# Performance work log

Hardware: AMD Instinct MI355X
Metric: run time of the kernel (lower is better)

The kernel has to match this reference:

```python
import jax, jax.numpy as jnp
import numpy as np

N, E, F_IN, D, X_DIM, T_DIM = 5000, 80000, 32, 64, 3, 6
P1, P2, H = 256, 32, 256
LOG_SCALE = 1.4763057  # sqrt(c) * 1.4763057 with c=1; Euclidean logmap0 is identity
W_DATA, W_PDE, W_ENT = 1.0, 1.0, 1.0

def time_encode(t):
    k_lin = T_DIM // 2
    k_log = T_DIM - k_lin
    s_lin = 10.0 ** jnp.arange(2, 2 * T_DIM, 1, dtype=jnp.float32)
    s_log = 10.0 ** jnp.arange(-2, 2 * T_DIM, 1, dtype=jnp.float32)
    t_lin = (t / jnp.clip(s_lin, 1e-7))[:k_lin]
    t_log = jnp.log((t / jnp.clip(s_log, 1e-7))[:k_log] + 1.0)
    return jnp.concatenate([t_lin, t_log])

def _forward(x0, adj, t, y, W_enc, W_pool1, W_pool2, W_emb1, W_emb2, W1, b1, W2, b2):
    t0 = t[0]
    # ---- encode: encoder + Euclidean log-map scaling ----
    z_x = jnp.tanh(x0 @ W_enc)                      # [N, D+X_DIM]
    z = z_x[:, :-X_DIM] * LOG_SCALE                 # [N, D]
    x_sp = 0.0 * z_x[:, -X_DIM:]                    # eps = 0 as in encode()
    t_enc = time_encode(t0)                         # [T_DIM]
    tx = jnp.concatenate([t_enc[None, :] * jnp.ones((N, 1)), x_sp], axis=-1)  # [N, T_DIM+X_DIM]
    # ---- renorm: dense adjacency scatter + DiffPool-style coarsening ----
    A = jnp.zeros((N, N), dtype=x0.dtype).at[adj[0], adj[1]].set(1.0)
    x = z
    y_cur = y                                        # [1, N]
    z_r = z
    y_r = y
    loss_ent = 0.0
    for Wp, We in ((W_pool1, W_emb1), (W_pool2, W_emb2)):
        S = jax.nn.softmax((x @ Wp) * LOG_SCALE, axis=0)        # [m, n] soft assignment
        m, n = S.shape
        ze = jnp.tanh(A @ (x @ We))                             # GNN embed at this level
        x = jnp.einsum('ij,ik->jk', S, ze) * (n / m)            # pooled features [n, D]
        y_cur = jnp.einsum('ij,ki->kj', S, y_cur) * (n / m)     # pooled targets [1, n]
        A = jnp.einsum('ji,jk,kl->il', S, A, S)                 # S^T A S -> [n, n]
        z_r = jnp.concatenate([z_r, x], axis=0)
        y_r = jnp.concatenate([y_r, y_cur], axis=-1)
        loss_ent = loss_ent + jax.scipy.special.entr(S).mean()
    M = z_r.shape[0]                                 # N + P1 + P2
    tx_all = tx[0] * jnp.ones((M, 1))                # broadcast first row -> [M, T_DIM+X_DIM]
    # ---- decoder + val_grad_lap: nested jacfwd Hessian diagonal ----
    def decode(txz):
        h = jnp.tanh(txz @ W1 + b1)
        return h @ W2 + b2                           # [1]
    def vgl(tx_i, z_i):
        def f(tx_):
            u = decode(jnp.concatenate([tx_, z_i]))
            return u, u
        def vg(tx_):
            g, u = jax.jacfwd(f, has_aux=True)(tx_)
            return g, (g, u)
        g2, (g, u) = jax.jacfwd(vg, has_aux=True)(tx_i)  # [1, d, d]
        hess = jax.vmap(jnp.diag)(g2)                     # [1, d]
        lap = hess[:, 1:].sum(1)                          # [1]
        return u, g, lap
    u, grad, lap = jax.vmap(vgl)(tx_all, z_r)        # [M,1], [M,1,d], [M,1]
    red = u.sum(-1)                                   # reduction -> [M]
    loss_data = jnp.mean(jnp.square(red - y_r[0]))
    res = grad[:, 0, 0] - lap[:, 0]                   # heat-equation residual u_t - lap
    loss_pde = jnp.mean(jnp.square(res))
    return W_DATA * loss_data + W_PDE * loss_pde + W_ENT * loss_ent

def setup_inputs():
    key = jax.random.key(0)
    ks = jax.random.split(key, 13)
    d_tx = T_DIM + X_DIM
    return {
        'x0': jax.random.normal(ks[0], (N, F_IN), dtype=jnp.float32),
        'adj': jax.random.randint(ks[1], (2, E), 0, N),
        't': jax.random.uniform(ks[2], (1,), dtype=jnp.float32) * 100.0,
        'y': jax.random.normal(ks[3], (1, N), dtype=jnp.float32),
        'W_enc': 0.2 * jax.random.normal(ks[4], (F_IN, D + X_DIM), dtype=jnp.float32),
        'W_pool1': 0.2 * jax.random.normal(ks[5], (D, P1), dtype=jnp.float32),
        'W_pool2': 0.2 * jax.random.normal(ks[6], (D, P2), dtype=jnp.float32),
        'W_emb1': 0.1 * jax.random.normal(ks[7], (D, D), dtype=jnp.float32),
        'W_emb2': 0.1 * jax.random.normal(ks[8], (D, D), dtype=jnp.float32),
        'W1': 0.1 * jax.random.normal(ks[9], (d_tx + D, H), dtype=jnp.float32),
        'b1': 0.01 * jax.random.normal(ks[10], (H,), dtype=jnp.float32),
        'W2': 0.1 * jax.random.normal(ks[11], (H, 1), dtype=jnp.float32),
        'b2': jnp.zeros((1,), dtype=jnp.float32),
    }

def reference(x0, adj, t, y, W_enc, W_pool1, W_pool2, W_emb1, W_emb2, W1, b1, W2, b2):
    return _forward(x0, adj, t, y, W_enc, W_pool1, W_pool2, W_emb1, W_emb2, W1, b1, W2, b2)
```

## Files before the change

kernel.cpp:

```cpp
#include <hip/hip_runtime.h>
#include <math.h>

#define NN 5000
#define EE 80000
#define FIN 32
#define DD 64
#define XD 3
#define TD 6
#define PP1 256
#define PP2 32
#define HH 256
#define MM (NN + PP1 + PP2)
#define CAP 64
#define NTILES 79
#define LOG_SCALE 1.4763057f
#define Y2SCALE (256.f / 5000.f)

#define A2CH 40
#define X2CH 79

#define ACC_OFF   0u
#define CNT_OFF   64u
#define DEG_OFF   256u
#define Y2A_OFF   20256u
#define X2_OFF    21280u
#define A2_OFF    86816u
#define BM_OFF    348960u
#define ZERO_BYTES 3473960u
#define PART_OFF  348960u
#define XW2_OFF   760608u
#define S2_OFF    826144u
#define ZE2_OFF   858912u
#define X3_OFF    924448u
#define Y3_OFF    932640u
#define BUCK_OFF  3473984u
#define ZEP_OFF   4753984u
#define Z_OFF     6033984u
#define S1_OFF    7313984u
#define AS1_OFF   12433984u
#define CQ_OFF    17553984u
#define DRES_OFF  17556032u
#define PA2_OFF   17598336u
#define PX2_OFF   28084096u
#define WS_ROOMY  33261504u

__device__ __forceinline__ float bsum256(float v, float* red) {
    int t = threadIdx.x;
    red[t] = v; __syncthreads();
    #pragma unroll
    for (int o = 128; o > 0; o >>= 1) {
        if (t < o) red[t] += red[t + o];
        __syncthreads();
    }
    float r = red[0]; __syncthreads();
    return r;
}

__global__ __launch_bounds__(256) void stage0(
        const float* __restrict__ x0, const float* __restrict__ Wenc,
        float* __restrict__ z,
        const int* __restrict__ adj, unsigned int* __restrict__ mask,
        int* __restrict__ bucket, int* __restrict__ deg,
        const float* __restrict__ t, const float* __restrict__ W1,
        const float* __restrict__ b1, float* __restrict__ cq) {
    __shared__ float smem[FIN * DD + 4 * FIN];
    int b = blockIdx.x;
    int tid = threadIdx.x;
    if (b < 1250) {
        float (*wx)[DD] = (float(*)[DD])smem;
        float (*xr)[FIN] = (float(*)[FIN])(smem + FIN * DD);
        int i0 = b << 2;
        int j = tid & 63;
        #pragma unroll
        for (int m = 0; m < 8; ++m) {
            int k = (tid >> 6) + (m << 2);
            wx[k][j] = Wenc[k * (DD + XD) + j];
        }
        if (tid < 128) xr[tid >> 5][tid & 31] = x0[(i0 + (tid >> 5)) * FIN + (tid & 31)];
        __syncthreads();
        int r = tid >> 6;
        float s = 0.f;
        #pragma unroll
        for (int k = 0; k < FIN; ++k) s = fmaf(xr[r][k], wx[k][j], s);
        z[(i0 + r) * DD + j] = tanhf(s) * LOG_SCALE;
    } else if (b < 1563) {
        int e = (b - 1250) * 256 + tid;
        if (e < EE) {
            int i = adj[e], jj = adj[EE + e];
            unsigned int key = (unsigned int)(i * NN + jj);
            unsigned int bit = 1u << (key & 31u);
            unsigned int old = atomicOr(&mask[key >> 5], bit);
            if (!(old & bit)) {
                int slot = atomicAdd(&deg[i], 1);
                if (slot < CAP) bucket[i * CAP + slot] = jj;
            }
        }
    } else {
        float* te = smem;
        int h = tid;
        if (h == 0) {
            float t0 = t[0];
            te[0] = t0 / 1e2f;
            te[1] = t0 / 1e3f;
            te[2] = t0 / 1e4f;
            te[3] = logf(t0 * 100.f + 1.f);
            te[4] = logf(t0 * 10.f + 1.f);
            te[5] = logf(t0 + 1.f);
        }
        __syncthreads();
        float c = b1[h];
        #pragma unroll
        for (int j2 = 0; j2 < TD; ++j2) c = fmaf(te[j2], W1[j2 * HH + h], c);
        float q = 0.f;
        #pragma unroll
        for (int j2 = 1; j2 < TD + XD; ++j2) { float w = W1[j2 * HH + h]; q = fmaf(w, w, q); }
        cq[h] = c;
        cq[HH + h] = q;
    }
}

__global__ __launch_bounds__(256) void stage1(
        const float* __restrict__ z, const float* __restrict__ Wp1,
        float* __restrict__ S1, float* __restrict__ part,
        const int* __restrict__ bucket, const int* __restrict__ deg,
        const float* __restrict__ We1, float* __restrict__ zep) {
    __shared__ float smem[2 * 64 * 64];
    int b = blockIdx.x;
    int tid = threadIdx.x;
    if (b < NTILES * 4) {
        float (*sa)[64] = (float(*)[64])smem;
        float (*sb)[64] = (float(*)[64])(smem + 4096);
        int tm = (b >> 2) << 6;
        int tn = (b & 3) << 6;
        int r0 = tid >> 4, c0 = (tid & 15) << 2;
        const float4 zero4 = make_float4(0.f, 0.f, 0.f, 0.f);
        #pragma unroll
        for (int m = 0; m < 4; ++m) {
            int row = r0 + (m << 4);
            int gr = tm + row;
            *(float4*)&sa[row][c0] = (gr < NN) ? *(const float4*)&z[gr * DD + c0] : zero4;
            *(float4*)&sb[row][c0] = *(const float4*)&Wp1[row * PP1 + tn + c0];
        }
        __syncthreads();
        int tx = (tid & 15) << 2;
        int ty = (tid >> 4) << 2;
        float acc[4][4] = {};
        #pragma unroll
        for (int kk = 0; kk < 64; ++kk) {
            float a0 = sa[ty + 0][kk];
            float a1 = sa[ty + 1][kk];
            float a2 = sa[ty + 2][kk];
            float a3 = sa[ty + 3][kk];
            float4 bv = *(const float4*)&sb[kk][tx];
            acc[0][0] = fmaf(a0, bv.x, acc[0][0]);
            acc[0][1] = fmaf(a0, bv.y, acc[0][1]);
            acc[0][2] = fmaf(a0, bv.z, acc[0][2]);
            acc[0][3] = fmaf(a0, bv.w, acc[0][3]);
            acc[1][0] = fmaf(a1, bv.x, acc[1][0]);
            acc[1][1] = fmaf(a1, bv.y, acc[1][1]);
            acc[1][2] = fmaf(a1, bv.z, acc[1][2]);
            acc[1][3] = fmaf(a1, bv.w, acc[1][3]);
            acc[2][0] = fmaf(a2, bv.x, acc[2][0]);
            acc[2][1] = fmaf(a2, bv.y, acc[2][1]);
            acc[2][2] = fmaf(a2, bv.z, acc[2][2]);
            acc[2][3] = fmaf(a2, bv.w, acc[2][3]);
            acc[3][0] = fmaf(a3, bv.x, acc[3][0]);
            acc[3][1] = fmaf(a3, bv.y, acc[3][1]);
            acc[3][2] = fmaf(a3, bv.z, acc[3][2]);
            acc[3][3] = fmaf(a3, bv.w, acc[3][3]);
        }
        #pragma unroll
        for (int i2 = 0; i2 < 4; ++i2)
            #pragma unroll
            for (int j = 0; j < 4; ++j) acc[i2][j] *= LOG_SCALE;
        #pragma unroll
        for (int i2 = 0; i2 < 4; ++i2) {
            int gr = tm + ty + i2;
            if (gr < NN)
                *(float4*)&S1[gr * PP1 + tn + tx] =
                    make_float4(acc[i2][0], acc[i2][1], acc[i2][2], acc[i2][3]);
        }
        int nvalid = NN - (tm + ty);
        nvalid = (nvalid < 0) ? 0 : (nvalid > 4 ? 4 : nvalid);
        float vm[4], vs[4];
        #pragma unroll
        for (int j = 0; j < 4; ++j) {
            float m = -3.0e38f;
            #pragma unroll
            for (int i2 = 0; i2 < 4; ++i2) if (i2 < nvalid) m = fmaxf(m, acc[i2][j]);
            float s = 0.f;
            #pragma unroll
            for (int i2 = 0; i2 < 4; ++i2) if (i2 < nvalid) s += expf(acc[i2][j] - m);
            vm[j] = m; vs[j] = s;
        }
        __syncthreads();
        float* redm = smem;
        float* reds = smem + 1024;
        int g = tid >> 4;
        #pragma unroll
        for (int j = 0; j < 4; ++j) {
            redm[g * 64 + tx + j] = vm[j];
            reds[g * 64 + tx + j] = vs[j];
        }
        __syncthreads();
        if (tid < 64) {
            float M = -3.0e38f, S = 0.f;
            #pragma unroll
            for (int g2 = 0; g2 < 16; ++g2) {
                float m2 = redm[g2 * 64 + tid], s2 = reds[g2 * 64 + tid];
                float Mn = fmaxf(M, m2);
                S = S * expf(M - Mn) + s2 * expf(m2 - Mn);
                M = Mn;
            }
            int rt = tm >> 6;
            part[rt * 512 + tn + tid] = M;
            part[rt * 512 + 256 + tn + tid] = S;
        }
    } else {
        float (*zs)[DD] = (float(*)[DD])smem;
        int w = tid >> 6, d = tid & 63;
        int i = ((b - NTILES * 4) << 2) + w;
        int n = min(deg[i], CAP);
        const int* bk = bucket + i * CAP;
        float a0 = 0.f, a1 = 0.f, a2 = 0.f, a3 = 0.f;
        int s = 0;
        for (; s + 4 <= n; s += 4) {
            a0 += z[bk[s] * DD + d];
            a1 += z[bk[s + 1] * DD + d];
            a2 += z[bk[s + 2] * DD + d];
            a3 += z[bk[s + 3] * DD + d];
        }
        for (; s < n; ++s) a0 += z[bk[s] * DD + d];
        zs[w][d] = (a0 + a1) + (a2 + a3);
        __syncthreads();
        float acc = 0.f;
        #pragma unroll
        for (int k = 0; k < DD; ++k) acc = fmaf(zs[w][k], We1[k * DD + d], acc);
        zep[i * DD + d] = tanhf(acc);
    }
}

__global__ void smax_norm(float* __restrict__ S, const float* __restrict__ part,
                          const float* __restrict__ y, float* __restrict__ y2acc,
                          float* __restrict__ ent) {
    __shared__ float red[256];
    __shared__ float ybuf[4][64];
    __shared__ float cst[64];
    int rt = blockIdx.x % NTILES, ct = blockIdx.x / NTILES;
    int lc = threadIdx.x & 63, q = threadIdx.x >> 6;
    int c = (ct << 6) + lc;
    float M = -3.0e38f, Sv = 0.f;
    for (int ch = q; ch < NTILES; ch += 4) {
        float m2 = part[ch * 512 + c];
        float s2 = part[ch * 512 + 256 + c];
        float Mn = fmaxf(M, m2);
        Sv = Sv * expf(M - Mn) + s2 * expf(m2 - Mn);
        M = Mn;
    }
    red[threadIdx.x] = M; ybuf[q][lc] = Sv;
    __syncthreads();
    if (q == 0) {
        float Mm = red[lc], Ss = ybuf[0][lc];
        #pragma unroll
        for (int g = 1; g < 4; ++g) {
            float m2 = red[g * 64 + lc], s2 = ybuf[g][lc];
            float Mn = fmaxf(Mm, m2);
            Ss = Ss * expf(Mm - Mn) + s2 * expf(m2 - Mn);
            Mm = Mn;
        }
        cst[lc] = Mm + logf(Ss);
    }
    __syncthreads();
    float mxlns = cst[lc];
    float en = 0.f, ys = 0.f;
    #pragma unroll
    for (int k = 0; k < 16; ++k) {
        int r = (rt << 6) + (k << 2) + q;
        if (r < NN) {
            float v = S[r * PP1 + c];
            float s = expf(v - mxlns);
            S[r * PP1 + c] = s;
            en += s * (mxlns - v);
            ys = fmaf(s, y[r], ys);
        }
    }
    __syncthreads();
    ybuf[q][lc] = ys;
    en = bsum256(en, red);
    if (threadIdx.x == 0) atomicAdd(ent, en);
    if (q == 0) atomicAdd(&y2acc[c], ybuf[0][lc] + ybuf[1][lc] + ybuf[2][lc] + ybuf[3][lc]);
}

__global__ void gather_as(const int* __restrict__ bucket, const int* __restrict__ deg,
                          const float* __restrict__ S1, float* __restrict__ AS1) {
    int i = blockIdx.x, c = threadIdx.x;
    int n = min(deg[i], CAP);
    const int* bk = bucket + i * CAP;
    float a0 = 0.f, a1 = 0.f, a2 = 0.f, a3 = 0.f;
    int s = 0;
    for (; s + 4 <= n; s += 4) {
        a0 += S1[bk[s] * PP1 + c];
        a1 += S1[bk[s + 1] * PP1 + c];
        a2 += S1[bk[s + 2] * PP1 + c];
        a3 += S1[bk[s + 3] * PP1 + c];
    }
    for (; s < n; ++s) a0 += S1[bk[s] * PP1 + c];
    AS1[i * PP1 + c] = (a0 + a1) + (a2 + a3);
}

__global__ __launch_bounds__(256) void gemm_fused(
        const float* __restrict__ S1, const float* __restrict__ AS1,
        const float* __restrict__ zep, float* __restrict__ PA2, float* __restrict__ PX2) {
    __shared__ float sa[32][64];
    __shared__ float sb[32][64];
    int b = blockIdx.x;
    const float* B;
    float* dst;
    int tm, tn, k0, k1, NB;
    if (b < 640) {
        int tile = b & 15, chunk = b >> 4;
        tm = (tile >> 2) << 6; tn = (tile & 3) << 6;
        k0 = chunk * 128; k1 = min(k0 + 128, NN);
        B = AS1; NB = PP1;
        dst = PA2 + chunk * (PP1 * PP1);
    } else {
        int b2 = b - 640;
        int tile = b2 & 3, chunk = b2 >> 2;
        tm = tile << 6; tn = 0;
        k0 = chunk * 64; k1 = min(k0 + 64, NN);
        B = zep; NB = DD;
        dst = PX2 + chunk * (PP1 * DD);
    }
    int tid = threadIdx.x;
    int tx = (tid & 15) << 2;
    int ty = (tid >> 4) << 2;
    int r0 = tid >> 4, c0 = (tid & 15) << 2;
    int r1 = (tid + 256) >> 4, c1 = c0;
    float acc[4][4] = {};
    const float4 z4 = make_float4(0.f, 0.f, 0.f, 0.f);
    for (int kb = k0; kb < k1; kb += 32) {
        int ka0 = kb + r0, ka1 = kb + r1;
        *(float4*)&sa[r0][c0] = (ka0 < k1) ? *(const float4*)&S1[ka0 * PP1 + tm + c0] : z4;
        *(float4*)&sa[r1][c1] = (ka1 < k1) ? *(const float4*)&S1[ka1 * PP1 + tm + c1] : z4;
        *(float4*)&sb[r0][c0] = (ka0 < k1) ? *(const float4*)&B[ka0 * NB + tn + c0] : z4;
        *(float4*)&sb[r1][c1] = (ka1 < k1) ? *(const float4*)&B[ka1 * NB + tn + c1] : z4;
        __syncthreads();
        #pragma unroll
        for (int kk = 0; kk < 32; ++kk) {
            float4 av = *(const float4*)&sa[kk][ty];
            float4 bv = *(const float4*)&sb[kk][tx];
            acc[0][0] = fmaf(av.x, bv.x, acc[0][0]);
            acc[0][1] = fmaf(av.x, bv.y, acc[0][1]);
            acc[0][2] = fmaf(av.x, bv.z, acc[0][2]);
            acc[0][3] = fmaf(av.x, bv.w, acc[0][3]);
            acc[1][0] = fmaf(av.y, bv.x, acc[1][0]);
            acc[1][1] = fmaf(av.y, bv.y, acc[1][1]);
            acc[1][2] = fmaf(av.y, bv.z, acc[1][2]);
            acc[1][3] = fmaf(av.y, bv.w, acc[1][3]);
            acc[2][0] = fmaf(av.z, bv.x, acc[2][0]);
            acc[2][1] = fmaf(av.z, bv.y, acc[2][1]);
            acc[2][2] = fmaf(av.z, bv.z, acc[2][2]);
            acc[2][3] = fmaf(av.z, bv.w, acc[2][3]);
            acc[3][0] = fmaf(av.w, bv.x, acc[3][0]);
            acc[3][1] = fmaf(av.w, bv.y, acc[3][1]);
            acc[3][2] = fmaf(av.w, bv.z, acc[3][2]);
            acc[3][3] = fmaf(av.w, bv.w, acc[3][3]);
        }
        __syncthreads();
    }
    #pragma unroll
    for (int i = 0; i < 4; ++i)
        *(float4*)&dst[(tm + ty + i) * NB + tn + tx] =
            make_float4(acc[i][0], acc[i][1], acc[i][2], acc[i][3]);
}

__global__ void reduce_parts(const float* __restrict__ PA2, const float* __restrict__ PX2,
                             float* __restrict__ A2, float* __restrict__ x2) {
    int idx = blockIdx.x * 256 + threadIdx.x;
    if (idx < PP1 * PP1) {
        float s = 0.f;
        #pragma unroll 8
        for (int c = 0; c < A2CH; ++c) s += PA2[c * (PP1 * PP1) + idx];
        A2[idx] = s;
    } else {
        int e = idx - PP1 * PP1;
        float s = 0.f;
        #pragma unroll 8
        for (int c = 0; c < X2CH; ++c) s += PX2[c * (PP1 * DD) + e];
        x2[e] = s * Y2SCALE;
    }
}

__global__ void gemm_tn(const float* __restrict__ A, const float* __restrict__ B,
                        float* __restrict__ C, int M, int N, int K, int kchunk, float scale) {
    __shared__ float sa[32][64];
    __shared__ float sb[32][64];
    int tilesN = N >> 6;
    int tm = (blockIdx.x / tilesN) << 6;
    int tn = (blockIdx.x % tilesN) << 6;
    int k0 = blockIdx.y * kchunk;
    int k1 = min(k0 + kchunk, K);
    int tid = threadIdx.x;
    int tx = (tid & 15) << 2;
    int ty = (tid >> 4) << 2;
    float acc[4][4] = {};
    for (int kb = k0; kb < k1; kb += 32) {
        #pragma unroll
        for (int t = 0; t < 8; ++t) {
            int idx = tid + (t << 8);
            int r = idx >> 6, cc = idx & 63;
            int k = kb + r;
            sa[r][cc] = (k < k1) ? A[k * M + tm + cc] : 0.f;
            sb[r][cc] = (k < k1) ? B[k * N + tn + cc] : 0.f;
        }
        __syncthreads();
        #pragma unroll
        for (int kk = 0; kk < 32; ++kk) {
            float4 av = *(const float4*)&sa[kk][ty];
            float4 bv = *(const float4*)&sb[kk][tx];
            acc[0][0] = fmaf(av.x, bv.x, acc[0][0]);
            acc[0][1] = fmaf(av.x, bv.y, acc[0][1]);
            acc[0][2] = fmaf(av.x, bv.z, acc[0][2]);
            acc[0][3] = fmaf(av.x, bv.w, acc[0][3]);
            acc[1][0] = fmaf(av.y, bv.x, acc[1][0]);
            acc[1][1] = fmaf(av.y, bv.y, acc[1][1]);
            acc[1][2] = fmaf(av.y, bv.z, acc[1][2]);
            acc[1][3] = fmaf(av.y, bv.w, acc[1][3]);
            acc[2][0] = fmaf(av.z, bv.x, acc[2][0]);
            acc[2][1] = fmaf(av.z, bv.y, acc[2][1]);
            acc[2][2] = fmaf(av.z, bv.z, acc[2][2]);
            acc[2][3] = fmaf(av.z, bv.w, acc[2][3]);
            acc[3][0] = fmaf(av.w, bv.x, acc[3][0]);
            acc[3][1] = fmaf(av.w, bv.y, acc[3][1]);
            acc[3][2] = fmaf(av.w, bv.z, acc[3][2]);
            acc[3][3] = fmaf(av.w, bv.w, acc[3][3]);
        }
        __syncthreads();
    }
    #pragma unroll
    for (int i = 0; i < 4; ++i)
        #pragma unroll
        for (int j = 0; j < 4; ++j)
            atomicAdd(&C[(tm + ty + i) * N + tn + tx + j], acc[i][j] * scale);
}

__global__ void mm2_fused(const float* __restrict__ x2, const float* __restrict__ We2,
                          const float* __restrict__ Wp2, float* __restrict__ XW2,
                          float* __restrict__ S2) {
    int gid = blockIdx.x * 256 + threadIdx.x;
    if (gid < PP1 * DD) {
        int i = gid >> 6, j = gid & 63;
        float s = 0.f;
        #pragma unroll
        for (int k = 0; k < DD; ++k) s = fmaf(x2[i * DD + k], We2[k * DD + j], s);
        XW2[gid] = s;
    } else {
        int e = gid - PP1 * DD;
        int i = e >> 5, j = e & 31;
        float s = 0.f;
        #pragma unroll
        for (int k = 0; k < DD; ++k) s = fmaf(x2[i * DD + k], Wp2[k * PP2 + j], s);
        S2[e] = s * LOG_SCALE;
    }
}

__global__ void level2b(float* __restrict__ S2, float* __restrict__ ent,
                        const float* __restrict__ y2acc, float* __restrict__ y3,
                        const float* __restrict__ A2, const float* __restrict__ XW2,
                        float* __restrict__ ze2) {
    __shared__ float red[256];
    int t = threadIdx.x;
    if (blockIdx.x < PP2) {
        int p = blockIdx.x;
        float l = S2[t * PP2 + p];
        red[t] = l; __syncthreads();
        #pragma unroll
        for (int o = 128; o > 0; o >>= 1) {
            if (t < o) red[t] = fmaxf(red[t], red[t + o]);
            __syncthreads();
        }
        float mx = red[0]; __syncthreads();
        float ex = expf(l - mx);
        float sum = bsum256(ex, red);
        float lns = logf(sum), inv = 1.f / sum;
        float s = ex * inv;
        S2[t * PP2 + p] = s;
        float en = s * (mx + lns - l);
        float ys = s * y2acc[t];
        en = bsum256(en, red);
        ys = bsum256(ys, red);
        if (t == 0) {
            atomicAdd(ent, en);
            y3[p] = ys * ((32.f / 256.f) * Y2SCALE);
        }
    } else {
        int gid = (blockIdx.x - PP2) * 256 + t;
        int i = gid >> 6, j = gid & 63;
        const float* a = A2 + i * PP1;
        float s = 0.f;
        #pragma unroll 16
        for (int k = 0; k < PP1; ++k) s = fmaf(a[k], XW2[k * DD + j], s);
        ze2[gid] = tanhf(s);
    }
}

__global__ void pool_x3(const float* __restrict__ S2, const float* __restrict__ ze2,
                        float* __restrict__ x3) {
    __shared__ float pr[4][64];
    int j = blockIdx.x;
    int d = threadIdx.x & 63, q = threadIdx.x >> 6;
    float a = 0.f;
    #pragma unroll 4
    for (int i = q * 64; i < q * 64 + 64; ++i)
        a = fmaf(S2[i * PP2 + j], ze2[i * DD + d], a);
    pr[q][d] = a;
    __syncthreads();
    if (q == 0) x3[j * DD + d] = (pr[0][d] + pr[1][d] + pr[2][d] + pr[3][d]) * (32.f / 256.f);
}

__global__ __launch_bounds__(256) void decoder8(
        const float* __restrict__ z, const float* __restrict__ x2,
        const float* __restrict__ x3, const float* __restrict__ y,
        const float* __restrict__ y2acc, const float* __restrict__ y3,
        const float* __restrict__ W1, const float* __restrict__ W2,
        const float* __restrict__ b2, const float* __restrict__ cq,
        float* __restrict__ dres, int* __restrict__ cnt,
        const float* __restrict__ acc, float* __restrict__ out) {
    __shared__ float zr[8][DD];
    __shared__ float rw[8][3][4];
    __shared__ int lastflag;
    int t = threadIdx.x;
    int i0 = blockIdx.x << 3;
    #pragma unroll
    for (int e = t; e < 512; e += 256) {
        int r = e >> 6, d = e & 63;
        int i = i0 + r;
        float v;
        if (i < NN) v = z[i * DD + d];
        else if (i < NN + PP1) v = x2[(i - NN) * DD + d];
        else v = x3[(i - NN - PP1) * DD + d];
        zr[r][d] = v;
    }
    __syncthreads();
    int h = t;
    float c0 = cq[h];
    float a[8];
    #pragma unroll
    for (int r = 0; r < 8; ++r) a[r] = c0;
    #pragma unroll 8
    for (int k = 0; k < DD; ++k) {
        float w = W1[(TD + XD + k) * HH + h];
        #pragma unroll
        for (int r = 0; r < 8; ++r) a[r] = fmaf(zr[r][k], w, a[r]);
    }
    float w2h = W2[h], w1h = W1[h], qh = cq[HH + h];
    float pu[8], pg[8], pl[8];
    #pragma unroll
    for (int r = 0; r < 8; ++r) {
        float th = tanhf(a[r]);
        float g1 = 1.f - th * th;
        pu[r] = w2h * th;
        pg[r] = w2h * g1 * w1h;
        pl[r] = w2h * (-2.f * th * g1) * qh;
    }
    #pragma unroll
    for (int o = 32; o > 0; o >>= 1) {
        #pragma unroll
        for (int r = 0; r < 8; ++r) {
            pu[r] += __shfl_xor(pu[r], o);
            pg[r] += __shfl_xor(pg[r], o);
            pl[r] += __shfl_xor(pl[r], o);
        }
    }
    int wave = t >> 6, lane = t & 63;
    if (lane == 0) {
        #pragma unroll
        for (int r = 0; r < 8; ++r) {
            rw[r][0][wave] = pu[r];
            rw[r][1][wave] = pg[r];
            rw[r][2][wave] = pl[r];
        }
    }
    __syncthreads();
    if (t < 8) {
        int r = t, i = i0 + r;
        float su = rw[r][0][0] + rw[r][0][1] + rw[r][0][2] + rw[r][0][3];
        float sg = rw[r][1][0] + rw[r][1][1] + rw[r][1][2] + rw[r][1][3];
        float sl = rw[r][2][0] + rw[r][2][1] + rw[r][2][2] + rw[r][2][3];
        float u = su + b2[0];
        float yv = (i < NN) ? y[i]
                 : (i < NN + PP1) ? y2acc[i - NN] * Y2SCALE
                 : y3[i - NN - PP1];
        float du = u - yv;
        float res = sg - sl;
        dres[i * 2] = du * du;
        dres[i * 2 + 1] = res * res;
        __threadfence();
    }
    __syncthreads();
    if (t == 0) lastflag = atomicAdd(cnt, 1);
    __syncthreads();
    if (lastflag == (MM / 8) - 1) {
        __threadfence();
        float* red = (float*)zr;
        float sd = 0.f, sp = 0.f;
        for (int i = t; i < MM; i += 256) {
            sd += dres[i * 2];
            sp += dres[i * 2 + 1];
        }
        sd = bsum256(sd, red);
        sp = bsum256(sp, red);
        if (t == 0)
            out[0] = sd * (1.f / MM) + sp * (1.f / MM)
                   + acc[2] * (1.f / (float)(NN * PP1)) + acc[3] * (1.f / (float)(PP1 * PP2));
    }
}

extern "C" void kernel_launch(void* const* d_in, const int* in_sizes, int n_in,
                              void* d_out, int out_size, void* d_ws, size_t ws_size,
                              hipStream_t stream) {
    const float* x0   = (const float*)d_in[0];
    const int*   adj  = (const int*)d_in[1];
    const float* t    = (const float*)d_in[2];
    const float* y    = (const float*)d_in[3];
    const float* Wenc = (const float*)d_in[4];
    const float* Wp1  = (const float*)d_in[5];
    const float* Wp2  = (const float*)d_in[6];
    const float* We1  = (const float*)d_in[7];
    const float* We2  = (const float*)d_in[8];
    const float* W1   = (const float*)d_in[9];
    const float* b1   = (const float*)d_in[10];
    const float* W2   = (const float*)d_in[11];
    const float* b2   = (const float*)d_in[12];

    char* ws = (char*)d_ws;
    float* acc   = (float*)(ws + ACC_OFF);
    int*   cnt   = (int*)(ws + CNT_OFF);
    int*   deg   = (int*)(ws + DEG_OFF);
    float* y2acc = (float*)(ws + Y2A_OFF);
    float* x2    = (float*)(ws + X2_OFF);
    float* A2    = (float*)(ws + A2_OFF);
    unsigned int* mask = (unsigned int*)(ws + BM_OFF);
    float* part  = (float*)(ws + PART_OFF);
    float* XW2   = (float*)(ws + XW2_OFF);
    float* S2    = (float*)(ws + S2_OFF);
    float* ze2   = (float*)(ws + ZE2_OFF);
    float* x3    = (float*)(ws + X3_OFF);
    float* y3    = (float*)(ws + Y3_OFF);
    int*   buck  = (int*)(ws + BUCK_OFF);
    float* zep   = (float*)(ws + ZEP_OFF);
    float* z     = (float*)(ws + Z_OFF);
    float* S1    = (float*)(ws + S1_OFF);
    float* AS1   = (float*)(ws + AS1_OFF);
    float* cq    = (float*)(ws + CQ_OFF);
    float* dres  = (float*)(ws + DRES_OFF);
    float* PA2   = (float*)(ws + PA2_OFF);
    float* PX2   = (float*)(ws + PX2_OFF);

    hipMemsetAsync(ws, 0, ZERO_BYTES, stream);

    stage0<<<1564, 256, 0, stream>>>(x0, Wenc, z, adj, mask, buck, deg, t, W1, b1, cq);
    stage1<<<NTILES * 4 + NN / 4, 256, 0, stream>>>(z, Wp1, S1, part, buck, deg, We1, zep);
    smax_norm<<<NTILES * 4, 256, 0, stream>>>(S1, part, y, y2acc, &acc[2]);
    gather_as<<<NN, PP1, 0, stream>>>(buck, deg, S1, AS1);
    if (ws_size >= WS_ROOMY) {
        gemm_fused<<<640 + 316, 256, 0, stream>>>(S1, AS1, zep, PA2, PX2);
        reduce_parts<<<320, 256, 0, stream>>>(PA2, PX2, A2, x2);
    } else {
        gemm_tn<<<dim3(4, 32), 256, 0, stream>>>(S1, zep, x2, PP1, DD, NN, 157, Y2SCALE);
        gemm_tn<<<dim3(16, 16), 256, 0, stream>>>(S1, AS1, A2, PP1, PP1, NN, 313, 1.f);
    }
    mm2_fused<<<96, 256, 0, stream>>>(x2, We2, Wp2, XW2, S2);
    level2b<<<96, 256, 0, stream>>>(S2, &acc[3], y2acc, y3, A2, XW2, ze2);
    pool_x3<<<PP2, 256, 0, stream>>>(S2, ze2, x3);
    decoder8<<<MM / 8, 256, 0, stream>>>(z, x2, x3, y, y2acc, y3, W1, W2, b2, cq,
                                         dres, cnt, acc, (float*)d_out);
}
```

Before: 227.4 us.

## Fuse gather, GEMM, decoder and pooling stages into fewer multi-role kernels

Several kernels are merged into multi-role launches. The AS1 gather, x2 GEMM partials and decoder rows for the original nodes now share one launch, and the A2 reduction, level-2 matmuls and decoder rows for the pooled nodes are folded together. pool_x3 and the final decoder become one small tail kernel that computes x3 in shared memory and does the last-block loss reduction. The aim is to cut launch count and inter-kernel gaps, and to overlap decoder work for the 5000 base rows with the pooling GEMMs. In exchange, block roles are more heterogeneous and the 4-block tail is serial.

```diff
diff --git a/kernel.cpp b/kernel.cpp
--- a/kernel.cpp
+++ b/kernel.cpp
@@ -15,7 +15,6 @@
 #define NTILES 79
 #define LOG_SCALE 1.4763057f
 #define Y2SCALE (256.f / 5000.f)
-
 #define A2CH 40
 #define X2CH 79
 
@@ -31,7 +30,6 @@
 #define XW2_OFF   760608u
 #define S2_OFF    826144u
 #define ZE2_OFF   858912u
-#define X3_OFF    924448u
 #define Y3_OFF    932640u
 #define BUCK_OFF  3473984u
 #define ZEP_OFF   4753984u
@@ -56,294 +54,24 @@
     return r;
 }
 
-__global__ __launch_bounds__(256) void stage0(
-        const float* __restrict__ x0, const float* __restrict__ Wenc,
-        float* __restrict__ z,
-        const int* __restrict__ adj, unsigned int* __restrict__ mask,
-        int* __restrict__ bucket, int* __restrict__ deg,
-        const float* __restrict__ t, const float* __restrict__ W1,
-        const float* __restrict__ b1, float* __restrict__ cq) {
-    __shared__ float smem[FIN * DD + 4 * FIN];
-    int b = blockIdx.x;
-    int tid = threadIdx.x;
-    if (b < 1250) {
-        float (*wx)[DD] = (float(*)[DD])smem;
-        float (*xr)[FIN] = (float(*)[FIN])(smem + FIN * DD);
-        int i0 = b << 2;
-        int j = tid & 63;
-        #pragma unroll
-        for (int m = 0; m < 8; ++m) {
-            int k = (tid >> 6) + (m << 2);
-            wx[k][j] = Wenc[k * (DD + XD) + j];
-        }
-        if (tid < 128) xr[tid >> 5][tid & 31] = x0[(i0 + (tid >> 5)) * FIN + (tid & 31)];
-        __syncthreads();
-        int r = tid >> 6;
-        float s = 0.f;
-        #pragma unroll
-        for (int k = 0; k < FIN; ++k) s = fmaf(xr[r][k], wx[k][j], s);
-        z[(i0 + r) * DD + j] = tanhf(s) * LOG_SCALE;
-    } else if (b < 1563) {
-        int e = (b - 1250) * 256 + tid;
-        if (e < EE) {
-            int i = adj[e], jj = adj[EE + e];
-            unsigned int key = (unsigned int)(i * NN + jj);
-            unsigned int bit = 1u << (key & 31u);
-            unsigned int old = atomicOr(&mask[key >> 5], bit);
-            if (!(old & bit)) {
-                int slot = atomicAdd(&deg[i], 1);
-                if (slot < CAP) bucket[i * CAP + slot] = jj;
-            }
-        }
-    } else {
-        float* te = smem;
-        int h = tid;
-        if (h == 0) {
-            float t0 = t[0];
-            te[0] = t0 / 1e2f;
-            te[1] = t0 / 1e3f;
-            te[2] = t0 / 1e4f;
-            te[3] = logf(t0 * 100.f + 1.f);
-            te[4] = logf(t0 * 10.f + 1.f);
-            te[5] = logf(t0 + 1.f);
-        }
-        __syncthreads();
-        float c = b1[h];
-        #pragma unroll
-        for (int j2 = 0; j2 < TD; ++j2) c = fmaf(te[j2], W1[j2 * HH + h], c);
-        float q = 0.f;
-        #pragma unroll
-        for (int j2 = 1; j2 < TD + XD; ++j2) { float w = W1[j2 * HH + h]; q = fmaf(w, w, q); }
-        cq[h] = c;
-        cq[HH + h] = q;
-    }
-}
-
-__global__ __launch_bounds__(256) void stage1(
-        const float* __restrict__ z, const float* __restrict__ Wp1,
-        float* __restrict__ S1, float* __restrict__ part,
-        const int* __restrict__ bucket, const int* __restrict__ deg,
-        const float* __restrict__ We1, float* __restrict__ zep) {
-    __shared__ float smem[2 * 64 * 64];
-    int b = blockIdx.x;
-    int tid = threadIdx.x;
-    if (b < NTILES * 4) {
-        float (*sa)[64] = (float(*)[64])smem;
-        float (*sb)[64] = (float(*)[64])(smem + 4096);
-        int tm = (b >> 2) << 6;
-        int tn = (b & 3) << 6;
-        int r0 = tid >> 4, c0 = (tid & 15) << 2;
-        const float4 zero4 = make_float4(0.f, 0.f, 0.f, 0.f);
-        #pragma unroll
-        for (int m = 0; m < 4; ++m) {
-            int row = r0 + (m << 4);
-            int gr = tm + row;
-            *(float4*)&sa[row][c0] = (gr < NN) ? *(const float4*)&z[gr * DD + c0] : zero4;
-            *(float4*)&sb[row][c0] = *(const float4*)&Wp1[row * PP1 + tn + c0];
-        }
-        __syncthreads();
-        int tx = (tid & 15) << 2;
-        int ty = (tid >> 4) << 2;
-        float acc[4][4] = {};
-        #pragma unroll
-        for (int kk = 0; kk < 64; ++kk) {
-            float a0 = sa[ty + 0][kk];
-            float a1 = sa[ty + 1][kk];
-            float a2 = sa[ty + 2][kk];
-            float a3 = sa[ty + 3][kk];
-            float4 bv = *(const float4*)&sb[kk][tx];
-            acc[0][0] = fmaf(a0, bv.x, acc[0][0]);
-            acc[0][1] = fmaf(a0, bv.y, acc[0][1]);
-            acc[0][2] = fmaf(a0, bv.z, acc[0][2]);
-            acc[0][3] = fmaf(a0, bv.w, acc[0][3]);
-            acc[1][0] = fmaf(a1, bv.x, acc[1][0]);
-            acc[1][1] = fmaf(a1, bv.y, acc[1][1]);
-            acc[1][2] = fmaf(a1, bv.z, acc[1][2]);
-            acc[1][3] = fmaf(a1, bv.w, acc[1][3]);
-            acc[2][0] = fmaf(a2, bv.x, acc[2][0]);
-            acc[2][1] = fmaf(a2, bv.y, acc[2][1]);
-            acc[2][2] = fmaf(a2, bv.z, acc[2][2]);
-            acc[2][3] = fmaf(a2, bv.w, acc[2][3]);
-            acc[3][0] = fmaf(a3, bv.x, acc[3][0]);
-            acc[3][1] = fmaf(a3, bv.y, acc[3][1]);
-            acc[3][2] = fmaf(a3, bv.z, acc[3][2]);
-            acc[3][3] = fmaf(a3, bv.w, acc[3][3]);
-        }
-        #pragma unroll
-        for (int i2 = 0; i2 < 4; ++i2)
-            #pragma unroll
-            for (int j = 0; j < 4; ++j) acc[i2][j] *= LOG_SCALE;
-        #pragma unroll
-        for (int i2 = 0; i2 < 4; ++i2) {
-            int gr = tm + ty + i2;
-            if (gr < NN)
-                *(float4*)&S1[gr * PP1 + tn + tx] =
-                    make_float4(acc[i2][0], acc[i2][1], acc[i2][2], acc[i2][3]);
-        }
-        int nvalid = NN - (tm + ty);
-        nvalid = (nvalid < 0) ? 0 : (nvalid > 4 ? 4 : nvalid);
-        float vm[4], vs[4];
-        #pragma unroll
-        for (int j = 0; j < 4; ++j) {
-            float m = -3.0e38f;
-            #pragma unroll
-            for (int i2 = 0; i2 < 4; ++i2) if (i2 < nvalid) m = fmaxf(m, acc[i2][j]);
-            float s = 0.f;
-            #pragma unroll
-            for (int i2 = 0; i2 < 4; ++i2) if (i2 < nvalid) s += expf(acc[i2][j] - m);
-            vm[j] = m; vs[j] = s;
-        }
-        __syncthreads();
-        float* redm = smem;
-        float* reds = smem + 1024;
-        int g = tid >> 4;
-        #pragma unroll
-        for (int j = 0; j < 4; ++j) {
-            redm[g * 64 + tx + j] = vm[j];
-            reds[g * 64 + tx + j] = vs[j];
-        }
-        __syncthreads();
-        if (tid < 64) {
-            float M = -3.0e38f, S = 0.f;
-            #pragma unroll
-            for (int g2 = 0; g2 < 16; ++g2) {
-                float m2 = redm[g2 * 64 + tid], s2 = reds[g2 * 64 + tid];
-                float Mn = fmaxf(M, m2);
-                S = S * expf(M - Mn) + s2 * expf(m2 - Mn);
-                M = Mn;
-            }
-            int rt = tm >> 6;
-            part[rt * 512 + tn + tid] = M;
-            part[rt * 512 + 256 + tn + tid] = S;
-        }
-    } else {
-        float (*zs)[DD] = (float(*)[DD])smem;
-        int w = tid >> 6, d = tid & 63;
-        int i = ((b - NTILES * 4) << 2) + w;
-        int n = min(deg[i], CAP);
-        const int* bk = bucket + i * CAP;
-        float a0 = 0.f, a1 = 0.f, a2 = 0.f, a3 = 0.f;
-        int s = 0;
-        for (; s + 4 <= n; s += 4) {
-            a0 += z[bk[s] * DD + d];
-            a1 += z[bk[s + 1] * DD + d];
-            a2 += z[bk[s + 2] * DD + d];
-            a3 += z[bk[s + 3] * DD + d];
-        }
-        for (; s < n; ++s) a0 += z[bk[s] * DD + d];
-        zs[w][d] = (a0 + a1) + (a2 + a3);
-        __syncthreads();
-        float acc = 0.f;
-        #pragma unroll
-        for (int k = 0; k < DD; ++k) acc = fmaf(zs[w][k], We1[k * DD + d], acc);
-        zep[i * DD + d] = tanhf(acc);
-    }
-}
-
-__global__ void smax_norm(float* __restrict__ S, const float* __restrict__ part,
-                          const float* __restrict__ y, float* __restrict__ y2acc,
-                          float* __restrict__ ent) {
-    __shared__ float red[256];
-    __shared__ float ybuf[4][64];
-    __shared__ float cst[64];
-    int rt = blockIdx.x % NTILES, ct = blockIdx.x / NTILES;
-    int lc = threadIdx.x & 63, q = threadIdx.x >> 6;
-    int c = (ct << 6) + lc;
-    float M = -3.0e38f, Sv = 0.f;
-    for (int ch = q; ch < NTILES; ch += 4) {
-        float m2 = part[ch * 512 + c];
-        float s2 = part[ch * 512 + 256 + c];
-        float Mn = fmaxf(M, m2);
-        Sv = Sv * expf(M - Mn) + s2 * expf(m2 - Mn);
-        M = Mn;
-    }
-    red[threadIdx.x] = M; ybuf[q][lc] = Sv;
-    __syncthreads();
-    if (q == 0) {
-        float Mm = red[lc], Ss = ybuf[0][lc];
-        #pragma unroll
-        for (int g = 1; g < 4; ++g) {
-            float m2 = red[g * 64 + lc], s2 = ybuf[g][lc];
-            float Mn = fmaxf(Mm, m2);
-            Ss = Ss * expf(Mm - Mn) + s2 * expf(m2 - Mn);
-            Mm = Mn;
-        }
-        cst[lc] = Mm + logf(Ss);
-    }
-    __syncthreads();
-    float mxlns = cst[lc];
-    float en = 0.f, ys = 0.f;
-    #pragma unroll
-    for (int k = 0; k < 16; ++k) {
-        int r = (rt << 6) + (k << 2) + q;
-        if (r < NN) {
-            float v = S[r * PP1 + c];
-            float s = expf(v - mxlns);
-            S[r * PP1 + c] = s;
-            en += s * (mxlns - v);
-            ys = fmaf(s, y[r], ys);
-        }
-    }
-    __syncthreads();
-    ybuf[q][lc] = ys;
-    en = bsum256(en, red);
-    if (threadIdx.x == 0) atomicAdd(ent, en);
-    if (q == 0) atomicAdd(&y2acc[c], ybuf[0][lc] + ybuf[1][lc] + ybuf[2][lc] + ybuf[3][lc]);
-}
-
-__global__ void gather_as(const int* __restrict__ bucket, const int* __restrict__ deg,
-                          const float* __restrict__ S1, float* __restrict__ AS1) {
-    int i = blockIdx.x, c = threadIdx.x;
-    int n = min(deg[i], CAP);
-    const int* bk = bucket + i * CAP;
-    float a0 = 0.f, a1 = 0.f, a2 = 0.f, a3 = 0.f;
-    int s = 0;
-    for (; s + 4 <= n; s += 4) {
-        a0 += S1[bk[s] * PP1 + c];
-        a1 += S1[bk[s + 1] * PP1 + c];
-        a2 += S1[bk[s + 2] * PP1 + c];
-        a3 += S1[bk[s + 3] * PP1 + c];
-    }
-    for (; s < n; ++s) a0 += S1[bk[s] * PP1 + c];
-    AS1[i * PP1 + c] = (a0 + a1) + (a2 + a3);
-}
-
-__global__ __launch_bounds__(256) void gemm_fused(
-        const float* __restrict__ S1, const float* __restrict__ AS1,
-        const float* __restrict__ zep, float* __restrict__ PA2, float* __restrict__ PX2) {
-    __shared__ float sa[32][64];
-    __shared__ float sb[32][64];
-    int b = blockIdx.x;
-    const float* B;
-    float* dst;
-    int tm, tn, k0, k1, NB;
-    if (b < 640) {
-        int tile = b & 15, chunk = b >> 4;
-        tm = (tile >> 2) << 6; tn = (tile & 3) << 6;
-        k0 = chunk * 128; k1 = min(k0 + 128, NN);
-        B = AS1; NB = PP1;
-        dst = PA2 + chunk * (PP1 * PP1);
-    } else {
-        int b2 = b - 640;
-        int tile = b2 & 3, chunk = b2 >> 2;
-        tm = tile << 6; tn = 0;
-        k0 = chunk * 64; k1 = min(k0 + 64, NN);
-        B = zep; NB = DD;
-        dst = PX2 + chunk * (PP1 * DD);
-    }
+__device__ void gemm_tile(const float* Amat, const float* Bmat,
+        int tm, int tn, int k0, int k1, int NB,
+        float* dst, int atomicMode, float scale, float* smem) {
+    float (*sa)[64] = (float(*)[64])smem;
+    float (*sb)[64] = (float(*)[64])(smem + 2048);
     int tid = threadIdx.x;
     int tx = (tid & 15) << 2;
     int ty = (tid >> 4) << 2;
     int r0 = tid >> 4, c0 = (tid & 15) << 2;
-    int r1 = (tid + 256) >> 4, c1 = c0;
+    int r1 = r0 + 16;
     float acc[4][4] = {};
     const float4 z4 = make_float4(0.f, 0.f, 0.f, 0.f);
     for (int kb = k0; kb < k1; kb += 32) {
         int ka0 = kb + r0, ka1 = kb + r1;
-        *(float4*)&sa[r0][c0] = (ka0 < k1) ? *(const float4*)&S1[ka0 * PP1 + tm + c0] : z4;
-        *(float4*)&sa[r1][c1] = (ka1 < k1) ? *(const float4*)&S1[ka1 * PP1 + tm + c1] : z4;
-        *(float4*)&sb[r0][c0] = (ka0 < k1) ? *(const float4*)&B[ka0 * NB + tn + c0] : z4;
-        *(float4*)&sb[r1][c1] = (ka1 < k1) ? *(const float4*)&B[ka1 * NB + tn + c1] : z4;
+        *(float4*)&sa[r0][c0] = (ka0 < k1) ? *(const float4*)&Amat[ka0 * PP1 + tm + c0] : z4;
+        *(float4*)&sa[r1][c0] = (ka1 < k1) ? *(const float4*)&Amat[ka1 * PP1 + tm + c0] : z4;
+        *(float4*)&sb[r0][c0] = (ka0 < k1) ? *(const float4*)&Bmat[ka0 * NB + tn + c0] : z4;
+        *(float4*)&sb[r1][c0] = (ka1 < k1) ? *(const float4*)&Bmat[ka1 * NB + tn + c0] : z4;
         __syncthreads();
         #pragma unroll
         for (int kk = 0; kk < 32; ++kk) {
@@ -368,106 +96,428 @@
         }
         __syncthreads();
     }
+    if (atomicMode) {
+        #pragma unroll
+        for (int i = 0; i < 4; ++i)
+            #pragma unroll
+            for (int j = 0; j < 4; ++j)
+                atomicAdd(&dst[(tm + ty + i) * NB + tn + tx + j], acc[i][j] * scale);
+    } else {
+        #pragma unroll
+        for (int i = 0; i < 4; ++i)
+            *(float4*)&dst[(tm + ty + i) * NB + tn + tx] =
+                make_float4(acc[i][0] * scale, acc[i][1] * scale,
+                            acc[i][2] * scale, acc[i][3] * scale);
+    }
+}
+
+__device__ void decoder_rows(const float* src, const float* ysrc, float yscale, int i0,
+        const float* W1, const float* W2, const float* b2, const float* cq,
+        float* dres, float* smem) {
+    float (*zr)[DD] = (float(*)[DD])smem;
+    float (*rw)[3][4] = (float(*)[3][4])(smem + 512);
+    int t = threadIdx.x;
+    zr[t >> 6][t & 63] = src[t];
+    zr[(t >> 6) + 4][t & 63] = src[t + 256];
+    __syncthreads();
+    int h = t;
+    float c0 = cq[h];
+    float a[8];
     #pragma unroll
-    for (int i = 0; i < 4; ++i)
-        *(float4*)&dst[(tm + ty + i) * NB + tn + tx] =
-            make_float4(acc[i][0], acc[i][1], acc[i][2], acc[i][3]);
-}
-
-__global__ void reduce_parts(const float* __restrict__ PA2, const float* __restrict__ PX2,
-                             float* __restrict__ A2, float* __restrict__ x2) {
-    int idx = blockIdx.x * 256 + threadIdx.x;
-    if (idx < PP1 * PP1) {
+    for (int r = 0; r < 8; ++r) a[r] = c0;
+    #pragma unroll 8
+    for (int k = 0; k < DD; ++k) {
+        float w = W1[(TD + XD + k) * HH + h];
+        #pragma unroll
+        for (int r = 0; r < 8; ++r) a[r] = fmaf(zr[r][k], w, a[r]);
+    }
+    float w2h = W2[h], w1h = W1[h], qh = cq[HH + h];
+    float pu[8], pg[8], pl[8];
+    #pragma unroll
+    for (int r = 0; r < 8; ++r) {
+        float th = tanhf(a[r]);
+        float g1 = 1.f - th * th;
+        pu[r] = w2h * th;
+        pg[r] = w2h * g1 * w1h;
+        pl[r] = w2h * (-2.f * th * g1) * qh;
+    }
+    #pragma unroll
+    for (int o = 32; o > 0; o >>= 1) {
+        #pragma unroll
+        for (int r = 0; r < 8; ++r) {
+            pu[r] += __shfl_xor(pu[r], o);
+            pg[r] += __shfl_xor(pg[r], o);
+            pl[r] += __shfl_xor(pl[r], o);
+        }
+    }
+    int wave = t >> 6, lane = t & 63;
+    if (lane == 0) {
+        #pragma unroll
+        for (int r = 0; r < 8; ++r) {
+            rw[r][0][wave] = pu[r];
+            rw[r][1][wave] = pg[r];
+            rw[r][2][wave] = pl[r];
+        }
+    }
+    __syncthreads();
+    if (t < 8) {
+        int r = t;
+        float su = rw[r][0][0] + rw[r][0][1] + rw[r][0][2] + rw[r][0][3];
+        float sg = rw[r][1][0] + rw[r][1][1] + rw[r][1][2] + rw[r][1][3];
+        float sl = rw[r][2][0] + rw[r][2][1] + rw[r][2][2] + rw[r][2][3];
+        float u = su + b2[0];
+        float du = u - ysrc[r] * yscale;
+        float res = sg - sl;
+        dres[(i0 + r) * 2] = du * du;
+        dres[(i0 + r) * 2 + 1] = res * res;
+    }
+    __syncthreads();
+}
+
+__global__ __launch_bounds__(256) void stage0(
+        const float* __restrict__ x0, const float* __restrict__ Wenc,
+        float* __restrict__ z,
+        const int* __restrict__ adj, unsigned int* __restrict__ mask,
+        int* __restrict__ bucket, int* __restrict__ deg,
+        const float* __restrict__ t, const float* __restrict__ W1,
+        const float* __restrict__ b1, float* __restrict__ cq) {
+    __shared__ __align__(16) float smem[FIN * DD + 4 * FIN];
+    int b = blockIdx.x;
+    int tid = threadIdx.x;
+    if (b < 1250) {
+        float (*wx)[DD] = (float(*)[DD])smem;
+        float (*xr)[FIN] = (float(*)[FIN])(smem + FIN * DD);
+        int i0 = b << 2;
+        int j = tid & 63;
+        #pragma unroll
+        for (int m = 0; m < 8; ++m) {
+            int k = (tid >> 6) + (m << 2);
+            wx[k][j] = Wenc[k * (DD + XD) + j];
+        }
+        if (tid < 128) xr[tid >> 5][tid & 31] = x0[(i0 + (tid >> 5)) * FIN + (tid & 31)];
+        __syncthreads();
+        int r = tid >> 6;
+        float s = 0.f;
+        #pragma unroll
+        for (int k = 0; k < FIN; ++k) s = fmaf(xr[r][k], wx[k][j], s);
+        z[(i0 + r) * DD + j] = tanhf(s) * LOG_SCALE;
+    } else if (b < 1563) {
+        int e = (b - 1250) * 256 + tid;
+        if (e < EE) {
+            int i = adj[e], jj = adj[EE + e];
+            unsigned int key = (unsigned int)(i * NN + jj);
+            unsigned int bit = 1u << (key & 31u);
+            unsigned int old = atomicOr(&mask[key >> 5], bit);
+            if (!(old & bit)) {
+                int slot = atomicAdd(&deg[i], 1);
+                if (slot < CAP) bucket[i * CAP + slot] = jj;
+            }
+        }
+    } else {
+        float* te = smem;
+        if (tid == 0) {
+            float t0 = t[0];
+            te[0] = t0 / 1e2f;
+            te[1] = t0 / 1e3f;
+            te[2] = t0 / 1e4f;
+            te[3] = logf(t0 * 100.f + 1.f);
+            te[4] = logf(t0 * 10.f + 1.f);
+            te[5] = logf(t0 + 1.f);
+        }
+        __syncthreads();
+        int h = tid;
+        float c = b1[h];
+        #pragma unroll
+        for (int j2 = 0; j2 < TD; ++j2) c = fmaf(te[j2], W1[j2 * HH + h], c);
+        float q = 0.f;
+        #pragma unroll
+        for (int j2 = 1; j2 < TD + XD; ++j2) { float w = W1[j2 * HH + h]; q = fmaf(w, w, q); }
+        cq[h] = c;
+        cq[HH + h] = q;
+    }
+}
+
+__global__ __launch_bounds__(256) void stage1(
+        const float* __restrict__ z, const float* __restrict__ Wp1,
+        float* __restrict__ S1, float* __restrict__ part,
+        const int* __restrict__ bucket, const int* __restrict__ deg,
+        const float* __restrict__ We1, float* __restrict__ zep) {
+    __shared__ __align__(16) float smem[2 * 64 * 64];
+    int b = blockIdx.x;
+    int tid = threadIdx.x;
+    if (b < NTILES * 4) {
+        float (*sa)[64] = (float(*)[64])smem;
+        float (*sb)[64] = (float(*)[64])(smem + 4096);
+        int tm = (b >> 2) << 6;
+        int tn = (b & 3) << 6;
+        int r0 = tid >> 4, c0 = (tid & 15) << 2;
+        const float4 zero4 = make_float4(0.f, 0.f, 0.f, 0.f);
+        #pragma unroll
+        for (int m = 0; m < 4; ++m) {
+            int row = r0 + (m << 4);
+            int gr = tm + row;
+            *(float4*)&sa[row][c0] = (gr < NN) ? *(const float4*)&z[gr * DD + c0] : zero4;
+            *(float4*)&sb[row][c0] = *(const float4*)&Wp1[row * PP1 + tn + c0];
+        }
+        __syncthreads();
+        int tx = (tid & 15) << 2;
+        int ty = (tid >> 4) << 2;
+        float acr[4][4] = {};
+        #pragma unroll
+        for (int kk = 0; kk < 64; ++kk) {
+            float a0 = sa[ty + 0][kk];
+            float a1 = sa[ty + 1][kk];
+            float a2 = sa[ty + 2][kk];
+            float a3 = sa[ty + 3][kk];
+            float4 bv = *(const float4*)&sb[kk][tx];
+            acr[0][0] = fmaf(a0, bv.x, acr[0][0]);
+            acr[0][1] = fmaf(a0, bv.y, acr[0][1]);
+            acr[0][2] = fmaf(a0, bv.z, acr[0][2]);
+            acr[0][3] = fmaf(a0, bv.w, acr[0][3]);
+            acr[1][0] = fmaf(a1, bv.x, acr[1][0]);
+            acr[1][1] = fmaf(a1, bv.y, acr[1][1]);
+            acr[1][2] = fmaf(a1, bv.z, acr[1][2]);
+            acr[1][3] = fmaf(a1, bv.w, acr[1][3]);
+            acr[2][0] = fmaf(a2, bv.x, acr[2][0]);
+            acr[2][1] = fmaf(a2, bv.y, acr[2][1]);
+            acr[2][2] = fmaf(a2, bv.z, acr[2][2]);
+            acr[2][3] = fmaf(a2, bv.w, acr[2][3]);
+            acr[3][0] = fmaf(a3, bv.x, acr[3][0]);
+            acr[3][1] = fmaf(a3, bv.y, acr[3][1]);
+            acr[3][2] = fmaf(a3, bv.z, acr[3][2]);
+            acr[3][3] = fmaf(a3, bv.w, acr[3][3]);
+        }
+        #pragma unroll
+        for (int i2 = 0; i2 < 4; ++i2)
+            #pragma unroll
+            for (int j = 0; j < 4; ++j) acr[i2][j] *= LOG_SCALE;
+        #pragma unroll
+        for (int i2 = 0; i2 < 4; ++i2) {
+            int gr = tm + ty + i2;
+            if (gr < NN)
+                *(float4*)&S1[gr * PP1 + tn + tx] =
+                    make_float4(acr[i2][0], acr[i2][1], acr[i2][2], acr[i2][3]);
+        }
+        int nvalid = NN - (tm + ty);
+        nvalid = (nvalid < 0) ? 0 : (nvalid > 4 ? 4 : nvalid);
+        float vm[4], vs[4];
+        #pragma unroll
+        for (int j = 0; j < 4; ++j) {
+            float m = -3.0e38f;
+            #pragma unroll
+            for (int i2 = 0; i2 < 4; ++i2) if (i2 < nvalid) m = fmaxf(m, acr[i2][j]);
+            float s = 0.f;
+            #pragma unroll
+            for (int i2 = 0; i2 < 4; ++i2) if (i2 < nvalid) s += expf(acr[i2][j] - m);
+            vm[j] = m; vs[j] = s;
+        }
+        __syncthreads();
+        float* redm = smem;
+        float* reds = smem + 1024;
+        int g = tid >> 4;
+        #pragma unroll
+        for (int j = 0; j < 4; ++j) {
+            redm[g * 64 + tx + j] = vm[j];
+            reds[g * 64 + tx + j] = vs[j];
+        }
+        __syncthreads();
+        if (tid < 64) {
+            float M = -3.0e38f, S = 0.f;
+            #pragma unroll
+            for (int g2 = 0; g2 < 16; ++g2) {
+                float m2 = redm[g2 * 64 + tid], s2 = reds[g2 * 64 + tid];
+                float Mn = fmaxf(M, m2);
+                S = S * expf(M - Mn) + s2 * expf(m2 - Mn);
+                M = Mn;
+            }
+            int rt = tm >> 6;
+            part[rt * 512 + tn + tid] = M;
+            part[rt * 512 + 256 + tn + tid] = S;
+        }
+    } else {
+        float (*zs)[DD] = (float(*)[DD])smem;
+        int w = tid >> 6, d = tid & 63;
+        int i = ((b - NTILES * 4) << 2) + w;
+        int n = min(deg[i], CAP);
+        const int* bk = bucket + i * CAP;
+        float a0 = 0.f, a1 = 0.f, a2 = 0.f, a3 = 0.f;
+        int s = 0;
+        for (; s + 4 <= n; s += 4) {
+            a0 += z[bk[s] * DD + d];
+            a1 += z[bk[s + 1] * DD + d];
+            a2 += z[bk[s + 2] * DD + d];
+            a3 += z[bk[s + 3] * DD + d];
+        }
+        for (; s < n; ++s) a0 += z[bk[s] * DD + d];
+        zs[w][d] = (a0 + a1) + (a2 + a3);
+        __syncthreads();
+        float a = 0.f;
+        #pragma unroll
+        for (int k = 0; k < DD; ++k) a = fmaf(zs[w][k], We1[k * DD + d], a);
+        zep[i * DD + d] = tanhf(a);
+    }
+}
+
+__global__ __launch_bounds__(256) void smax_norm(
+        float* __restrict__ S, const float* __restrict__ part,
+        const float* __restrict__ y, float* __restrict__ y2acc,
+        float* __restrict__ ent) {
+    __shared__ float red[256];
+    __shared__ float ybuf[4][64];
+    __shared__ float cst[64];
+    int rt = blockIdx.x % NTILES, ct = blockIdx.x / NTILES;
+    int lc = threadIdx.x & 63, q = threadIdx.x >> 6;
+    int c = (ct << 6) + lc;
+    float M = -3.0e38f, Sv = 0.f;
+    for (int ch = q; ch < NTILES; ch += 4) {
+        float m2 = part[ch * 512 + c];
+        float s2 = part[ch * 512 + 256 + c];
+        float Mn = fmaxf(M, m2);
+        Sv = Sv * expf(M - Mn) + s2 * expf(m2 - Mn);
+        M = Mn;
+    }
+    red[threadIdx.x] = M; ybuf[q][lc] = Sv;
+    __syncthreads();
+    if (q == 0) {
+        float Mm = red[lc], Ss = ybuf[0][lc];
+        #pragma unroll
+        for (int g = 1; g < 4; ++g) {
+            float m2 = red[g * 64 + lc], s2 = ybuf[g][lc];
+            float Mn = fmaxf(Mm, m2);
+            Ss = Ss * expf(Mm - Mn) + s2 * expf(m2 - Mn);
+            Mm = Mn;
+        }
+        cst[lc] = Mm + logf(Ss);
+    }
+    __syncthreads();
+    float mxlns = cst[lc];
+    float en = 0.f, ys = 0.f;
+    #pragma unroll
+    for (int k = 0; k < 16; ++k) {
+        int r = (rt << 6) + (k << 2) + q;
+        if (r < NN) {
+            float v = S[r * PP1 + c];
+            float s = expf(v - mxlns);
+            S[r * PP1 + c] = s;
+            en += s * (mxlns - v);
+            ys = fmaf(s, y[r], ys);
+        }
+    }
+    __syncthreads();
+    ybuf[q][lc] = ys;
+    en = bsum256(en, red);
+    if (threadIdx.x == 0) atomicAdd(ent, en);
+    if (q == 0) atomicAdd(&y2acc[c], ybuf[0][lc] + ybuf[1][lc] + ybuf[2][lc] + ybuf[3][lc]);
+}
+
+__global__ __launch_bounds__(256) void fuseD(
+        const int* __restrict__ bucket, const int* __restrict__ deg,
+        const float* __restrict__ S1, float* __restrict__ AS1,
+        const float* __restrict__ zep, float* __restrict__ PX2,
+        float* __restrict__ x2,
+        const float* __restrict__ z, const float* __restrict__ y,
+        const float* __restrict__ W1, const float* __restrict__ W2,
+        const float* __restrict__ b2, const float* __restrict__ cq,
+        float* __restrict__ dres, int roomy) {
+    __shared__ __align__(16) float smem[4096];
+    int b = blockIdx.x;
+    if (b < NN) {
+        int i = b, c = threadIdx.x;
+        int n = min(deg[i], CAP);
+        const int* bk = bucket + i * CAP;
+        float a0 = 0.f, a1 = 0.f, a2 = 0.f, a3 = 0.f;
+        int s = 0;
+        for (; s + 4 <= n; s += 4) {
+            a0 += S1[bk[s] * PP1 + c];
+            a1 += S1[bk[s + 1] * PP1 + c];
+            a2 += S1[bk[s + 2] * PP1 + c];
+            a3 += S1[bk[s + 3] * PP1 + c];
+        }
+        for (; s < n; ++s) a0 += S1[bk[s] * PP1 + c];
+        AS1[i * PP1 + c] = (a0 + a1) + (a2 + a3);
+    } else if (b < NN + 316) {
+        int vb2 = b - NN;
+        int tile = vb2 & 3, chunk = vb2 >> 2;
+        int k0 = chunk * 64, k1 = min(k0 + 64, NN);
+        float* dst = roomy ? (PX2 + chunk * (PP1 * DD)) : x2;
+        gemm_tile(S1, zep, tile << 6, 0, k0, k1, DD, dst, 1 - roomy,
+                  roomy ? 1.f : Y2SCALE, smem);
+    } else {
+        int r8 = b - (NN + 316);
+        decoder_rows(z + (r8 << 3) * DD, y + (r8 << 3), 1.f, r8 << 3,
+                     W1, W2, b2, cq, dres, smem);
+    }
+}
+
+__global__ __launch_bounds__(256) void fuseE(
+        const float* __restrict__ S1, const float* __restrict__ AS1,
+        float* __restrict__ PA2, float* __restrict__ A2,
+        const float* __restrict__ PX2, float* __restrict__ x2, int roomy) {
+    __shared__ __align__(16) float smem[4096];
+    int b = blockIdx.x;
+    if (b < 640) {
+        int tile = b & 15, chunk = b >> 4;
+        int k0 = chunk * 128, k1 = min(k0 + 128, NN);
+        float* dst = roomy ? (PA2 + chunk * (PP1 * PP1)) : A2;
+        gemm_tile(S1, AS1, (tile >> 2) << 6, (tile & 3) << 6, k0, k1, PP1,
+                  dst, 1 - roomy, 1.f, smem);
+    } else if (roomy) {
+        int idx = (b - 640) * 256 + threadIdx.x;
         float s = 0.f;
         #pragma unroll 8
-        for (int c = 0; c < A2CH; ++c) s += PA2[c * (PP1 * PP1) + idx];
-        A2[idx] = s;
+        for (int c = 0; c < X2CH; ++c) s += PX2[c * (PP1 * DD) + idx];
+        x2[idx] = s * Y2SCALE;
+    }
+}
+
+__global__ __launch_bounds__(256) void fuseF(
+        const float* __restrict__ PA2, float* __restrict__ A2,
+        const float* __restrict__ x2, const float* __restrict__ We2,
+        const float* __restrict__ Wp2, float* __restrict__ XW2,
+        float* __restrict__ S2,
+        const float* __restrict__ y2acc,
+        const float* __restrict__ W1, const float* __restrict__ W2,
+        const float* __restrict__ b2, const float* __restrict__ cq,
+        float* __restrict__ dres, int roomy) {
+    __shared__ __align__(16) float smem[640];
+    int b = blockIdx.x;
+    int tid = threadIdx.x;
+    if (b < 256) {
+        if (roomy) {
+            int idx = b * 256 + tid;
+            float s = 0.f;
+            #pragma unroll 8
+            for (int c = 0; c < A2CH; ++c) s += PA2[c * (PP1 * PP1) + idx];
+            A2[idx] = s;
+        }
+    } else if (b < 352) {
+        int gid = (b - 256) * 256 + tid;
+        if (gid < PP1 * DD) {
+            int i = gid >> 6, j = gid & 63;
+            float s = 0.f;
+            #pragma unroll
+            for (int k = 0; k < DD; ++k) s = fmaf(x2[i * DD + k], We2[k * DD + j], s);
+            XW2[gid] = s;
+        } else {
+            int e = gid - PP1 * DD;
+            int i = e >> 5, j = e & 31;
+            float s = 0.f;
+            #pragma unroll
+            for (int k = 0; k < DD; ++k) s = fmaf(x2[i * DD + k], Wp2[k * PP2 + j], s);
+            S2[e] = s * LOG_SCALE;
+        }
     } else {
-        int e = idx - PP1 * PP1;
-        float s = 0.f;
-        #pragma unroll 8
-        for (int c = 0; c < X2CH; ++c) s += PX2[c * (PP1 * DD) + e];
-        x2[e] = s * Y2SCALE;
-    }
-}
-
-__global__ void gemm_tn(const float* __restrict__ A, const float* __restrict__ B,
-                        float* __restrict__ C, int M, int N, int K, int kchunk, float scale) {
-    __shared__ float sa[32][64];
-    __shared__ float sb[32][64];
-    int tilesN = N >> 6;
-    int tm = (blockIdx.x / tilesN) << 6;
-    int tn = (blockIdx.x % tilesN) << 6;
-    int k0 = blockIdx.y * kchunk;
-    int k1 = min(k0 + kchunk, K);
-    int tid = threadIdx.x;
-    int tx = (tid & 15) << 2;
-    int ty = (tid >> 4) << 2;
-    float acc[4][4] = {};
-    for (int kb = k0; kb < k1; kb += 32) {
-        #pragma unroll
-        for (int t = 0; t < 8; ++t) {
-            int idx = tid + (t << 8);
-            int r = idx >> 6, cc = idx & 63;
-            int k = kb + r;
-            sa[r][cc] = (k < k1) ? A[k * M + tm + cc] : 0.f;
-            sb[r][cc] = (k < k1) ? B[k * N + tn + cc] : 0.f;
-        }
-        __syncthreads();
-        #pragma unroll
-        for (int kk = 0; kk < 32; ++kk) {
-            float4 av = *(const float4*)&sa[kk][ty];
-            float4 bv = *(const float4*)&sb[kk][tx];
-            acc[0][0] = fmaf(av.x, bv.x, acc[0][0]);
-            acc[0][1] = fmaf(av.x, bv.y, acc[0][1]);
-            acc[0][2] = fmaf(av.x, bv.z, acc[0][2]);
-            acc[0][3] = fmaf(av.x, bv.w, acc[0][3]);
-            acc[1][0] = fmaf(av.y, bv.x, acc[1][0]);
-            acc[1][1] = fmaf(av.y, bv.y, acc[1][1]);
-            acc[1][2] = fmaf(av.y, bv.z, acc[1][2]);
-            acc[1][3] = fmaf(av.y, bv.w, acc[1][3]);
-            acc[2][0] = fmaf(av.z, bv.x, acc[2][0]);
-            acc[2][1] = fmaf(av.z, bv.y, acc[2][1]);
-            acc[2][2] = fmaf(av.z, bv.z, acc[2][2]);
-            acc[2][3] = fmaf(av.z, bv.w, acc[2][3]);
-            acc[3][0] = fmaf(av.w, bv.x, acc[3][0]);
-            acc[3][1] = fmaf(av.w, bv.y, acc[3][1]);
-            acc[3][2] = fmaf(av.w, bv.z, acc[3][2]);
-            acc[3][3] = fmaf(av.w, bv.w, acc[3][3]);
-        }
-        __syncthreads();
-    }
-    #pragma unroll
-    for (int i = 0; i < 4; ++i)
-        #pragma unroll
-        for (int j = 0; j < 4; ++j)
-            atomicAdd(&C[(tm + ty + i) * N + tn + tx + j], acc[i][j] * scale);
-}
-
-__global__ void mm2_fused(const float* __restrict__ x2, const float* __restrict__ We2,
-                          const float* __restrict__ Wp2, float* __restrict__ XW2,
-                          float* __restrict__ S2) {
-    int gid = blockIdx.x * 256 + threadIdx.x;
-    if (gid < PP1 * DD) {
-        int i = gid >> 6, j = gid & 63;
-        float s = 0.f;
-        #pragma unroll
-        for (int k = 0; k < DD; ++k) s = fmaf(x2[i * DD + k], We2[k * DD + j], s);
-        XW2[gid] = s;
-    } else {
-        int e = gid - PP1 * DD;
-        int i = e >> 5, j = e & 31;
-        float s = 0.f;
-        #pragma unroll
-        for (int k = 0; k < DD; ++k) s = fmaf(x2[i * DD + k], Wp2[k * PP2 + j], s);
-        S2[e] = s * LOG_SCALE;
-    }
-}
-
-__global__ void level2b(float* __restrict__ S2, float* __restrict__ ent,
-                        const float* __restrict__ y2acc, float* __restrict__ y3,
-                        const float* __restrict__ A2, const float* __restrict__ XW2,
-                        float* __restrict__ ze2) {
+        int r8 = b - 352;
+        decoder_rows(x2 + (r8 << 3) * DD, y2acc + (r8 << 3), Y2SCALE, NN + (r8 << 3),
+                     W1, W2, b2, cq, dres, smem);
+    }
+}
+
+__global__ __launch_bounds__(256) void fuseH(
+        float* __restrict__ S2, float* __restrict__ ent,
+        const float* __restrict__ y2acc, float* __restrict__ y3,
+        const float* __restrict__ A2, const float* __restrict__ XW2,
+        float* __restrict__ ze2) {
     __shared__ float red[256];
     int t = threadIdx.x;
     if (blockIdx.x < PP2) {
@@ -504,105 +554,37 @@
     }
 }
 
-__global__ void pool_x3(const float* __restrict__ S2, const float* __restrict__ ze2,
-                        float* __restrict__ x3) {
-    __shared__ float pr[4][64];
-    int j = blockIdx.x;
-    int d = threadIdx.x & 63, q = threadIdx.x >> 6;
-    float a = 0.f;
-    #pragma unroll 4
-    for (int i = q * 64; i < q * 64 + 64; ++i)
-        a = fmaf(S2[i * PP2 + j], ze2[i * DD + d], a);
-    pr[q][d] = a;
-    __syncthreads();
-    if (q == 0) x3[j * DD + d] = (pr[0][d] + pr[1][d] + pr[2][d] + pr[3][d]) * (32.f / 256.f);
-}
-
-__global__ __launch_bounds__(256) void decoder8(
-        const float* __restrict__ z, const float* __restrict__ x2,
-        const float* __restrict__ x3, const float* __restrict__ y,
-        const float* __restrict__ y2acc, const float* __restrict__ y3,
+__global__ __launch_bounds__(256) void tail(
+        const float* __restrict__ S2, const float* __restrict__ ze2,
+        const float* __restrict__ y3,
         const float* __restrict__ W1, const float* __restrict__ W2,
         const float* __restrict__ b2, const float* __restrict__ cq,
         float* __restrict__ dres, int* __restrict__ cnt,
         const float* __restrict__ acc, float* __restrict__ out) {
-    __shared__ float zr[8][DD];
-    __shared__ float rw[8][3][4];
+    __shared__ __align__(16) float smem[1152];
     __shared__ int lastflag;
     int t = threadIdx.x;
-    int i0 = blockIdx.x << 3;
+    int jbase = blockIdx.x << 3;
     #pragma unroll
-    for (int e = t; e < 512; e += 256) {
-        int r = e >> 6, d = e & 63;
-        int i = i0 + r;
-        float v;
-        if (i < NN) v = z[i * DD + d];
-        else if (i < NN + PP1) v = x2[(i - NN) * DD + d];
-        else v = x3[(i - NN - PP1) * DD + d];
-        zr[r][d] = v;
-    }
-    __syncthreads();
-    int h = t;
-    float c0 = cq[h];
-    float a[8];
-    #pragma unroll
-    for (int r = 0; r < 8; ++r) a[r] = c0;
-    #pragma unroll 8
-    for (int k = 0; k < DD; ++k) {
-        float w = W1[(TD + XD + k) * HH + h];
-        #pragma unroll
-        for (int r = 0; r < 8; ++r) a[r] = fmaf(zr[r][k], w, a[r]);
-    }
-    float w2h = W2[h], w1h = W1[h], qh = cq[HH + h];
-    float pu[8], pg[8], pl[8];
-    #pragma unroll
-    for (int r = 0; r < 8; ++r) {
-        float th = tanhf(a[r]);
-        float g1 = 1.f - th * th;
-        pu[r] = w2h * th;
-        pg[r] = w2h * g1 * w1h;
-        pl[r] = w2h * (-2.f * th * g1) * qh;
-    }
-    #pragma unroll
-    for (int o = 32; o > 0; o >>= 1) {
-        #pragma unroll
-        for (int r = 0; r < 8; ++r) {
-            pu[r] += __shfl_xor(pu[r], o);
-            pg[r] += __shfl_xor(pg[r], o);
-            pl[r] += __shfl_xor(pl[r], o);
-        }
-    }
-    int wave = t >> 6, lane = t & 63;
-    if (lane == 0) {
-        #pragma unroll
-        for (int r = 0; r < 8; ++r) {
-            rw[r][0][wave] = pu[r];
-            rw[r][1][wave] = pg[r];
-            rw[r][2][wave] = pl[r];
-        }
-    }
-    __syncthreads();
-    if (t < 8) {
-        int r = t, i = i0 + r;
-        float su = rw[r][0][0] + rw[r][0][1] + rw[r][0][2] + rw[r][0][3];
-        float sg = rw[r][1][0] + rw[r][1][1] + rw[r][1][2] + rw[r][1][3];
-        float sl = rw[r][2][0] + rw[r][2][1] + rw[r][2][2] + rw[r][2][3];
-        float u = su + b2[0];
-        float yv = (i < NN) ? y[i]
-                 : (i < NN + PP1) ? y2acc[i - NN] * Y2SCALE
-                 : y3[i - NN - PP1];
-        float du = u - yv;
-        float res = sg - sl;
-        dres[i * 2] = du * du;
-        dres[i * 2 + 1] = res * res;
+    for (int kk = 0; kk < 2; ++kk) {
+        int idx = t + kk * 256;
+        int jl = idx >> 6, d = idx & 63;
+        int j = jbase + jl;
+        float a = 0.f;
+        for (int i = 0; i < PP1; ++i)
+            a = fmaf(S2[i * PP2 + j], ze2[i * DD + d], a);
+        smem[idx] = a * (32.f / 256.f);
+    }
+    __syncthreads();
+    decoder_rows(smem, y3 + jbase, 1.f, NN + PP1 + jbase,
+                 W1, W2, b2, cq, dres, smem + 512);
+    if (t < 8) __threadfence();
+    __syncthreads();
+    if (t == 0) lastflag = atomicAdd(cnt, 1);
+    __syncthreads();
+    if (lastflag == 3) {
         __threadfence();
-    }
-    __syncthreads();
-    if (t == 0) lastflag = atomicAdd(cnt, 1);
-    __syncthreads();
-    if (lastflag == (MM / 8) - 1) {
-        __threadfence();
-        float* red = (float*)zr;
+        float* red = smem;
         float sd = 0.f, sp = 0.f;
         for (int i = t; i < MM; i += 256) {
             sd += dres[i * 2];
@@ -645,7 +627,6 @@
     float* XW2   = (float*)(ws + XW2_OFF);
     float* S2    = (float*)(ws + S2_OFF);
     float* ze2   = (float*)(ws + ZE2_OFF);
-    float* x3    = (float*)(ws + X3_OFF);
     float* y3    = (float*)(ws + Y3_OFF);
     int*   buck  = (int*)(ws + BUCK_OFF);
     float* zep   = (float*)(ws + ZEP_OFF);
@@ -656,23 +637,19 @@
     float* dres  = (float*)(ws + DRES_OFF);
     float* PA2   = (float*)(ws + PA2_OFF);
     float* PX2   = (float*)(ws + PX2_OFF);
+    int roomy = (ws_size >= WS_ROOMY) ? 1 : 0;
 
     hipMemsetAsync(ws, 0, ZERO_BYTES, stream);
 
     stage0<<<1564, 256, 0, stream>>>(x0, Wenc, z, adj, mask, buck, deg, t, W1, b1, cq);
     stage1<<<NTILES * 4 + NN / 4, 256, 0, stream>>>(z, Wp1, S1, part, buck, deg, We1, zep);
     smax_norm<<<NTILES * 4, 256, 0, stream>>>(S1, part, y, y2acc, &acc[2]);
-    gather_as<<<NN, PP1, 0, stream>>>(buck, deg, S1, AS1);
-    if (ws_size >= WS_ROOMY) {
-        gemm_fused<<<640 + 316, 256, 0, stream>>>(S1, AS1, zep, PA2, PX2);
-        reduce_parts<<<320, 256, 0, stream>>>(PA2, PX2, A2, x2);
-    } else {
-        gemm_tn<<<dim3(4, 32), 256, 0, stream>>>(S1, zep, x2, PP1, DD, NN, 157, Y2SCALE);
-        gemm_tn<<<dim3(16, 16), 256, 0, stream>>>(S1, AS1, A2, PP1, PP1, NN, 313, 1.f);
-    }
-    mm2_fused<<<96, 256, 0, stream>>>(x2, We2, Wp2, XW2, S2);
-    level2b<<<96, 256, 0, stream>>>(S2, &acc[3], y2acc, y3, A2, XW2, ze2);
-    pool_x3<<<PP2, 256, 0, stream>>>(S2, ze2, x3);
-    decoder8<<<MM / 8, 256, 0, stream>>>(z, x2, x3, y, y2acc, y3, W1, W2, b2, cq,
-                                         dres, cnt, acc, (float*)d_out);
-}
+    fuseD<<<NN + 316 + 625, 256, 0, stream>>>(buck, deg, S1, AS1, zep, PX2, x2,
+                                              z, y, W1, W2, b2, cq, dres, roomy);
+    fuseE<<<704, 256, 0, stream>>>(S1, AS1, PA2, A2, PX2, x2, roomy);
+    fuseF<<<384, 256, 0, stream>>>(PA2, A2, x2, We2, Wp2, XW2, S2, y2acc,
+                                   W1, W2, b2, cq, dres, roomy);
+    fuseH<<<96, 256, 0, stream>>>(S2, &acc[3], y2acc, y3, A2, XW2, ze2);
+    tail<<<4, 256, 0, stream>>>(S2, ze2, y3, W1, W2, b2, cq,
+                                dres, cnt, acc, (float*)d_out);
+}
```

Result: slower. 325.2 us (+43.0%).
